# Optimization experiments

Hardware: AMD Instinct MI355X
Metric: run time of the kernel (lower is better)

## Reference

```python
import jax, jax.numpy as jnp
import numpy as np

D_MODEL = 1024
D_STATE = 16
DT_RANK = 64  # ceil(1024/16)
DT_MIN, DT_MAX = 1e-3, 1e-1


def setup_inputs() -> dict:
    key = jax.random.key(0)
    ks = jax.random.split(key, 6)
    x = jax.random.normal(ks[0], (2, 2048, D_MODEL), jnp.float32)
    A_log = jax.random.normal(ks[1], (D_MODEL, D_STATE), jnp.float32)
    D = jax.random.normal(ks[2], (D_MODEL,), jnp.float32)
    # nn.Linear default init ~ U(-1/sqrt(fan_in), 1/sqrt(fan_in)); normal*scale is fine for a baseline
    x_proj_w = jax.random.normal(ks[3], (DT_RANK + 2 * D_STATE, D_MODEL), jnp.float32) * (D_MODEL ** -0.5)
    dt_init_std = DT_RANK ** -0.5
    dt_proj_w = jax.random.uniform(ks[4], (D_MODEL, DT_RANK), jnp.float32, -dt_init_std, dt_init_std)
    dt = jnp.exp(jax.random.uniform(ks[5], (D_MODEL,), jnp.float32)
                 * (np.log(DT_MAX) - np.log(DT_MIN)) + np.log(DT_MIN))
    dt_proj_b = dt + jnp.log(-jnp.expm1(-dt))  # inverse-softplus init
    return {"x": x, "A_log": A_log, "D": D, "x_proj_w": x_proj_w,
            "dt_proj_w": dt_proj_w, "dt_proj_b": dt_proj_b}


def _s6(x, A_log, D, x_proj_w, dt_proj_w, dt_proj_b):
    A = -jnp.exp(A_log)                                    # (d, n)
    xp = jnp.einsum('bld,ed->ble', x, x_proj_w)            # (b, l, r+2n)
    d_rank = xp[..., :DT_RANK]
    Bm = xp[..., DT_RANK:DT_RANK + D_STATE]                # (b, l, n)
    Cm = xp[..., DT_RANK + D_STATE:]                       # (b, l, n)
    delta = jax.nn.softplus(jnp.einsum('blr,dr->bld', d_rank, dt_proj_w) + dt_proj_b)
    deltaA = jnp.exp(jnp.einsum('bld,dn->bldn', delta, A))          # (b, l, d, n)
    deltaB_u = jnp.einsum('bld,bln,bld->bldn', delta, Bm, x)        # (b, l, d, n)

    def step(h, inp):
        dA_t, dBu_t, C_t = inp          # (b,d,n), (b,d,n), (b,n)
        h = dA_t * h + dBu_t
        y = jnp.einsum('bdn,bn->bd', h, C_t)
        return h, y

    b, l, d = x.shape
    h0 = jnp.zeros((b, d, D_STATE), x.dtype)
    _, ys = jax.lax.scan(step, h0,
                         (deltaA.transpose(1, 0, 2, 3),
                          deltaB_u.transpose(1, 0, 2, 3),
                          Cm.transpose(1, 0, 2)))
    y = ys.transpose(1, 0, 2) + x * D                      # (b, l, d)
    return y


def reference(x, A_log, D, x_proj_w, dt_proj_w, dt_proj_b):
    return _s6(x, A_log, D, x_proj_w, dt_proj_w, dt_proj_b)
```

## Files before the change

### kernel.cpp

```cpp
#include <hip/hip_runtime.h>
#include <math.h>

#define Bb 2
#define Ll 2048
#define Dm 1024
#define Ns 16
#define Rr 64
#define Ee 96
#define XPS 8
#define BLK (Bb*Ll)
#define NTHR 256
#define LOG2E 1.4426950408889634f
#define LN2   0.6931471805599453f

__device__ inline float ex2(float x) {
#if __has_builtin(__builtin_amdgcn_exp2f)
    return __builtin_amdgcn_exp2f(x);
#else
    return exp2f(x);
#endif
}
__device__ inline float lg2(float x) {
#if __has_builtin(__builtin_amdgcn_logf)
    return __builtin_amdgcn_logf(x);
#else
    return log2f(x);
#endif
}
__device__ inline float softplus_f(float z) {
    float e = ex2(-fabsf(z) * LOG2E);
    return fmaxf(z, 0.f) + lg2(1.f + e) * LN2;
}

__global__ void __launch_bounds__(NTHR)
k_xproj(const float* __restrict__ x, const float* __restrict__ xw,
        float* __restrict__ xp_part) {
    __shared__ __align__(16) float xs[32 * 68];
    __shared__ __align__(16) float wsh[32 * 100];
    int bx = blockIdx.x;
    int ks = bx & 7, mt = bx >> 3;
    int i0 = mt * 64;
    int tid = threadIdx.x;
    int tx = tid & 15, ty = tid >> 4;
    float acc[4][6];
#pragma unroll
    for (int ii = 0; ii < 4; ++ii)
#pragma unroll
        for (int jj = 0; jj < 6; ++jj) acc[ii][jj] = 0.f;

    for (int kc = 0; kc < 4; ++kc) {
        int k0 = ks * 128 + kc * 32;
        for (int t = tid; t < 512; t += NTHR) {
            int r = t >> 3, c = (t & 7) * 4;
            float4 v = *(const float4*)(x + (size_t)(i0 + r) * Dm + k0 + c);
            xs[(c+0)*68+r] = v.x; xs[(c+1)*68+r] = v.y;
            xs[(c+2)*68+r] = v.z; xs[(c+3)*68+r] = v.w;
        }
        for (int t = tid; t < 768; t += NTHR) {
            int r = t >> 3, c = (t & 7) * 4;
            float4 v = *(const float4*)(xw + (size_t)r * Dm + k0 + c);
            wsh[(c+0)*100+r] = v.x; wsh[(c+1)*100+r] = v.y;
            wsh[(c+2)*100+r] = v.z; wsh[(c+3)*100+r] = v.w;
        }
        __syncthreads();
#pragma unroll 8
        for (int k = 0; k < 32; ++k) {
            float4 xv = *(const float4*)(xs + k*68 + ty*4);
            float2 w0 = *(const float2*)(wsh + k*100 + tx*6 + 0);
            float2 w1 = *(const float2*)(wsh + k*100 + tx*6 + 2);
            float2 w2 = *(const float2*)(wsh + k*100 + tx*6 + 4);
            float xr[4] = {xv.x, xv.y, xv.z, xv.w};
            float wr[6] = {w0.x, w0.y, w1.x, w1.y, w2.x, w2.y};
#pragma unroll
            for (int ii = 0; ii < 4; ++ii)
#pragma unroll
                for (int jj = 0; jj < 6; ++jj)
                    acc[ii][jj] = fmaf(xr[ii], wr[jj], acc[ii][jj]);
        }
        __syncthreads();
    }
#pragma unroll
    for (int ii = 0; ii < 4; ++ii)
#pragma unroll
        for (int jj = 0; jj < 6; ++jj)
            xp_part[((size_t)ks * BLK + (i0 + ty*4 + ii)) * Ee + tx*6 + jj] = acc[ii][jj];
}

__global__ void __launch_bounds__(NTHR)
k_prep(const float* __restrict__ xp_part, float* __restrict__ xp) {
    int g = blockIdx.x * NTHR + threadIdx.x;
    const float4* p = (const float4*)xp_part;
    float4 s = p[g];
#pragma unroll
    for (int i = 1; i < XPS; ++i) {
        float4 v = p[(size_t)i * (BLK * Ee / 4) + g];
        s.x += v.x; s.y += v.y; s.z += v.z; s.w += v.w;
    }
    ((float4*)xp)[g] = s;
}

__global__ void __launch_bounds__(NTHR)
k_delta(const float* __restrict__ xp, const float* __restrict__ dtw,
        const float* __restrict__ dtb, float* __restrict__ delta) {
    __shared__ __align__(16) float xs[64 * 136];
    __shared__ __align__(16) float wsh[64 * 68];
    int bx = blockIdx.x;
    int nt = bx & 15, mt = bx >> 4;
    int i0 = mt * 128, j0 = nt * 64;
    int tid = threadIdx.x, tx = tid & 15, ty = tid >> 4;

    for (int t = tid; t < 2048; t += NTHR) {
        int r = t >> 4, c = (t & 15) * 4;
        float4 v = *(const float4*)(xp + (size_t)(i0 + r) * Ee + c);
        xs[(c+0)*136+r] = v.x; xs[(c+1)*136+r] = v.y;
        xs[(c+2)*136+r] = v.z; xs[(c+3)*136+r] = v.w;
    }
    for (int t = tid; t < 1024; t += NTHR) {
        int r = t >> 4, c = (t & 15) * 4;
        float4 w = *(const float4*)(dtw + (size_t)(j0 + r) * Rr + c);
        wsh[(c+0)*68+r] = w.x; wsh[(c+1)*68+r] = w.y;
        wsh[(c+2)*68+r] = w.z; wsh[(c+3)*68+r] = w.w;
    }
    __syncthreads();

    float acc[8][4];
#pragma unroll
    for (int ii = 0; ii < 8; ++ii)
#pragma unroll
        for (int jj = 0; jj < 4; ++jj) acc[ii][jj] = 0.f;
#pragma unroll 8
    for (int k = 0; k < 64; ++k) {
        float4 xa = *(const float4*)(xs + k*136 + ty*8 + 0);
        float4 xb = *(const float4*)(xs + k*136 + ty*8 + 4);
        float4 wv = *(const float4*)(wsh + k*68 + tx*4);
        float xr[8] = {xa.x,xa.y,xa.z,xa.w, xb.x,xb.y,xb.z,xb.w};
        float wr[4] = {wv.x, wv.y, wv.z, wv.w};
#pragma unroll
        for (int ii = 0; ii < 8; ++ii)
#pragma unroll
            for (int jj = 0; jj < 4; ++jj)
                acc[ii][jj] = fmaf(xr[ii], wr[jj], acc[ii][jj]);
    }
    int d0 = j0 + tx * 4;
    float4 bias = *(const float4*)(dtb + d0);
#pragma unroll
    for (int ii = 0; ii < 8; ++ii) {
        int bl = i0 + ty*8 + ii;
        float4 o;
        o.x = softplus_f(acc[ii][0] + bias.x);
        o.y = softplus_f(acc[ii][1] + bias.y);
        o.z = softplus_f(acc[ii][2] + bias.z);
        o.w = softplus_f(acc[ii][3] + bias.w);
        *(float4*)(delta + (size_t)bl * Dm + d0) = o;
    }
}

__device__ inline void load_a2(const float* __restrict__ A_log, int d, float* a2) {
    const float4* Ap = (const float4*)(A_log + (size_t)d * Ns);
    float4 a0 = Ap[0], a1 = Ap[1], a2v = Ap[2], a3 = Ap[3];
    float tmp[Ns] = {a0.x,a0.y,a0.z,a0.w, a1.x,a1.y,a1.z,a1.w,
                     a2v.x,a2v.y,a2v.z,a2v.w, a3.x,a3.y,a3.z,a3.w};
#pragma unroll
    for (int n = 0; n < Ns; ++n) a2[n] = -__expf(tmp[n]) * LOG2E;
}

template<int CHv>
__global__ void __launch_bounds__(NTHR)
k_scan_part(const float* __restrict__ delta, const float* __restrict__ x,
            const float* __restrict__ xp, const float* __restrict__ A_log,
            float* __restrict__ Ec, float* __restrict__ Sc) {
    constexpr int CLv = Ll / CHv;
    int bx = blockIdx.x;
    int dblk = bx & 3, chunk = (bx >> 2) & (CHv - 1), b = bx >> 2 >> __builtin_ctz(CHv);
    int tid = threadIdx.x;
    int d = dblk * 256 + tid;
    int row0 = b * Ll + chunk * CLv;

    float a2[Ns], h[Ns];
    load_a2(A_log, d, a2);
#pragma unroll
    for (int n = 0; n < Ns; ++n) h[n] = 0.f;
    float sd = 0.f;

#pragma unroll 4
    for (int t = 0; t < CLv; ++t) {
        size_t row = (size_t)(row0 + t);
        float dl = delta[row * Dm + d];
        float xv = x[row * Dm + d];
        const float* bp = xp + row * Ee + Rr;
        float4 B0 = *(const float4*)(bp + 0),  B1 = *(const float4*)(bp + 4);
        float4 B2 = *(const float4*)(bp + 8),  B3 = *(const float4*)(bp + 12);
        float Bv[Ns] = {B0.x,B0.y,B0.z,B0.w, B1.x,B1.y,B1.z,B1.w,
                        B2.x,B2.y,B2.z,B2.w, B3.x,B3.y,B3.z,B3.w};
        float dx = dl * xv;
        sd += dl;
#pragma unroll
        for (int n = 0; n < Ns; ++n)
            h[n] = fmaf(ex2(dl * a2[n]), h[n], dx * Bv[n]);
    }
    size_t base = ((size_t)b * CHv + chunk) * Dm + d;
    float4* Ep = (float4*)(Ec + base * Ns);
    Ep[0] = make_float4(h[0],  h[1],  h[2],  h[3]);
    Ep[1] = make_float4(h[4],  h[5],  h[6],  h[7]);
    Ep[2] = make_float4(h[8],  h[9],  h[10], h[11]);
    Ep[3] = make_float4(h[12], h[13], h[14], h[15]);
    Sc[base] = sd;
}

template<int CHv, int G>
__global__ void __launch_bounds__(NTHR)
k_comb1(const float* __restrict__ Ec, const float* __restrict__ Sc,
        const float* __restrict__ A_log, float* __restrict__ Hloc,
        float* __restrict__ Spre, float* __restrict__ Eg, float* __restrict__ Sg) {
    constexpr int CPG = CHv / G;
    int gid = blockIdx.x * NTHR + threadIdx.x;
    int n = gid & (Ns - 1);
    int d = (gid >> 4) & (Dm - 1);
    int g = (gid >> 14) & (G - 1);
    int b = gid >> 17;
    float a2 = -__expf(A_log[d * Ns + n]) * LOG2E;
    float h = 0.f, S = 0.f;
#pragma unroll
    for (int j = 0; j < CPG; ++j) {
        size_t base = ((size_t)b * CHv + g * CPG + j) * Dm + d;
        float e  = Ec[base * Ns + n];
        float sc = Sc[base];
        Hloc[base * Ns + n] = h;
        if (n == 0) Spre[base] = S;
        h = fmaf(ex2(a2 * sc), h, e);
        S += sc;
    }
    size_t gb = ((size_t)b * G + g) * Dm + d;
    Eg[gb * Ns + n] = h;
    if (n == 0) Sg[gb] = S;
}

template<int G>
__global__ void __launch_bounds__(NTHR)
k_comb2(const float* __restrict__ Eg, const float* __restrict__ Sg,
        const float* __restrict__ A_log, float* __restrict__ Hg) {
    int gid = blockIdx.x * NTHR + threadIdx.x;
    int n = gid & (Ns - 1);
    int d = (gid >> 4) & (Dm - 1);
    int b = gid >> 14;
    float a2 = -__expf(A_log[d * Ns + n]) * LOG2E;
    float h = 0.f;
#pragma unroll
    for (int g = 0; g < G; ++g) {
        size_t gb = ((size_t)b * G + g) * Dm + d;
        Hg[gb * Ns + n] = h;
        h = fmaf(ex2(a2 * Sg[gb]), h, Eg[gb * Ns + n]);
    }
}

template<int CHv, int G>
__global__ void __launch_bounds__(NTHR)
k_scan_full(const float* __restrict__ delta, const float* __restrict__ x,
            const float* __restrict__ xp, const float* __restrict__ A_log,
            const float* __restrict__ Dp, const float* __restrict__ Hloc,
            const float* __restrict__ Spre, const float* __restrict__ Hg,
            float* __restrict__ out) {
    constexpr int CLv = Ll / CHv;
    constexpr int CPG = CHv / G;
    int bx = blockIdx.x;
    int dblk = bx & 3, chunk = (bx >> 2) & (CHv - 1), b = bx >> 2 >> __builtin_ctz(CHv);
    int tid = threadIdx.x;
    int d = dblk * 256 + tid;
    int row0 = b * Ll + chunk * CLv;

    float a2[Ns], h[Ns];
    load_a2(A_log, d, a2);
    size_t base = ((size_t)b * CHv + chunk) * Dm + d;
    size_t gb   = ((size_t)b * G + chunk / CPG) * Dm + d;
    {
        float sp = Spre[base];
        const float4* Hl = (const float4*)(Hloc + base * Ns);
        const float4* Hp = (const float4*)(Hg + gb * Ns);
        float4 l0 = Hl[0], l1 = Hl[1], l2 = Hl[2], l3 = Hl[3];
        float4 g0 = Hp[0], g1 = Hp[1], g2 = Hp[2], g3 = Hp[3];
        float lv[Ns] = {l0.x,l0.y,l0.z,l0.w, l1.x,l1.y,l1.z,l1.w,
                        l2.x,l2.y,l2.z,l2.w, l3.x,l3.y,l3.z,l3.w};
        float gv[Ns] = {g0.x,g0.y,g0.z,g0.w, g1.x,g1.y,g1.z,g1.w,
                        g2.x,g2.y,g2.z,g2.w, g3.x,g3.y,g3.z,g3.w};
#pragma unroll
        for (int n = 0; n < Ns; ++n) h[n] = fmaf(ex2(a2[n] * sp), gv[n], lv[n]);
    }
    float Dval = Dp[d];

#pragma unroll 4
    for (int t = 0; t < CLv; ++t) {
        size_t row = (size_t)(row0 + t);
        float dl = delta[row * Dm + d];
        float xv = x[row * Dm + d];
        const float* bp = xp + row * Ee + Rr;
        float4 B0 = *(const float4*)(bp + 0),  B1 = *(const float4*)(bp + 4);
        float4 B2 = *(const float4*)(bp + 8),  B3 = *(const float4*)(bp + 12);
        float4 C0 = *(const float4*)(bp + 16), C1 = *(const float4*)(bp + 20);
        float4 C2 = *(const float4*)(bp + 24), C3 = *(const float4*)(bp + 28);
        float Bv[Ns] = {B0.x,B0.y,B0.z,B0.w, B1.x,B1.y,B1.z,B1.w,
                        B2.x,B2.y,B2.z,B2.w, B3.x,B3.y,B3.z,B3.w};
        float Cv[Ns] = {C0.x,C0.y,C0.z,C0.w, C1.x,C1.y,C1.z,C1.w,
                        C2.x,C2.y,C2.z,C2.w, C3.x,C3.y,C3.z,C3.w};
        float dx = dl * xv;
        float ya[4] = {0.f, 0.f, 0.f, 0.f};
#pragma unroll
        for (int n = 0; n < Ns; ++n) {
            h[n] = fmaf(ex2(dl * a2[n]), h[n], dx * Bv[n]);
            ya[n & 3] = fmaf(h[n], Cv[n], ya[n & 3]);
        }
        out[row * Dm + d] = fmaf(xv, Dval, (ya[0] + ya[1]) + (ya[2] + ya[3]));
    }
}

extern "C" void kernel_launch(void* const* d_in, const int* in_sizes, int n_in,
                              void* d_out, int out_size, void* d_ws, size_t ws_size,
                              hipStream_t stream) {
    const float* x     = (const float*)d_in[0];
    const float* A_log = (const float*)d_in[1];
    const float* Dp    = (const float*)d_in[2];
    const float* xw    = (const float*)d_in[3];
    const float* dtw   = (const float*)d_in[4];
    const float* dtb   = (const float*)d_in[5];
    float* out = (float*)d_out;
    float* ws  = (float*)d_ws;

    float* xp      = ws;
    float* delta   = xp + 393216;
    float* S3      = delta + 4194304;
    float* xp_part = S3;

    k_xproj<<<dim3(512), dim3(NTHR), 0, stream>>>(x, xw, xp_part);
    k_prep <<<dim3(384), dim3(NTHR), 0, stream>>>(xp_part, xp);
    k_delta<<<dim3(512), dim3(NTHR), 0, stream>>>(xp, dtw, dtb, delta);

    constexpr int G = 8;
    size_t s3_128 = (size_t)Bb*128*Dm*Ns + (size_t)Bb*128*Dm + (size_t)Bb*128*Dm*Ns
                  + (size_t)Bb*128*Dm + (size_t)Bb*G*Dm*Ns + (size_t)Bb*G*Dm
                  + (size_t)Bb*G*Dm*Ns;
    size_t need128 = ((size_t)393216 + 4194304 + s3_128) * 4;
    if (ws_size >= need128) {
        constexpr int CHv = 128;
        float* Ec   = S3;
        float* Sc   = Ec   + (size_t)Bb*CHv*Dm*Ns;
        float* Hloc = Sc   + (size_t)Bb*CHv*Dm;
        float* Spre = Hloc + (size_t)Bb*CHv*Dm*Ns;
        float* Eg   = Spre + (size_t)Bb*CHv*Dm;
        float* Sg   = Eg   + (size_t)Bb*G*Dm*Ns;
        float* Hg   = Sg   + (size_t)Bb*G*Dm;
        k_scan_part<CHv>  <<<dim3(Bb*CHv*4), dim3(NTHR), 0, stream>>>(delta, x, xp, A_log, Ec, Sc);
        k_comb1<CHv, G>   <<<dim3(Bb*G*Dm*Ns/NTHR), dim3(NTHR), 0, stream>>>(Ec, Sc, A_log, Hloc, Spre, Eg, Sg);
        k_comb2<G>        <<<dim3(Bb*Dm*Ns/NTHR), dim3(NTHR), 0, stream>>>(Eg, Sg, A_log, Hg);
        k_scan_full<CHv,G><<<dim3(Bb*CHv*4), dim3(NTHR), 0, stream>>>(delta, x, xp, A_log, Dp, Hloc, Spre, Hg, out);
    } else {
        constexpr int CHv = 64;
        float* Ec   = S3;
        float* Sc   = Ec   + (size_t)Bb*CHv*Dm*Ns;
        float* Hloc = Sc   + (size_t)Bb*CHv*Dm;
        float* Spre = Hloc + (size_t)Bb*CHv*Dm*Ns;
        float* Eg   = Spre + (size_t)Bb*CHv*Dm;
        float* Sg   = Eg   + (size_t)Bb*G*Dm*Ns;
        float* Hg   = Sg   + (size_t)Bb*G*Dm;
        k_scan_part<CHv>  <<<dim3(Bb*CHv*4), dim3(NTHR), 0, stream>>>(delta, x, xp, A_log, Ec, Sc);
        k_comb1<CHv, G>   <<<dim3(Bb*G*Dm*Ns/NTHR), dim3(NTHR), 0, stream>>>(Ec, Sc, A_log, Hloc, Spre, Eg, Sg);
        k_comb2<G>        <<<dim3(Bb*Dm*Ns/NTHR), dim3(NTHR), 0, stream>>>(Eg, Sg, A_log, Hg);
        k_scan_full<CHv,G><<<dim3(Bb*CHv*4), dim3(NTHR), 0, stream>>>(delta, x, xp, A_log, Dp, Hloc, Spre, Hg, out);
    }
}
```

Measured before the change: 152.3 us.

## Fuse delta projection and softplus into both scan passes, drop delta buffer

Removes the separate k_delta GEMM kernel and the materialized delta tensor (B*L*D floats). Each scan thread now keeps its 64 dt_proj weights in registers and recomputes delta per timestep from the xp row, in both the partial and the full scan passes. This trades a 4M-float write and two reads of that tensor for twice the dot-product work and higher register pressure. The chunk count is also fixed at 64, where the code before chose 128 whenever the workspace was large enough.

```diff
diff --git a/kernel.cpp b/kernel.cpp
--- a/kernel.cpp
+++ b/kernel.cpp
@@ -99,62 +99,6 @@
     ((float4*)xp)[g] = s;
 }
 
-__global__ void __launch_bounds__(NTHR)
-k_delta(const float* __restrict__ xp, const float* __restrict__ dtw,
-        const float* __restrict__ dtb, float* __restrict__ delta) {
-    __shared__ __align__(16) float xs[64 * 136];
-    __shared__ __align__(16) float wsh[64 * 68];
-    int bx = blockIdx.x;
-    int nt = bx & 15, mt = bx >> 4;
-    int i0 = mt * 128, j0 = nt * 64;
-    int tid = threadIdx.x, tx = tid & 15, ty = tid >> 4;
-
-    for (int t = tid; t < 2048; t += NTHR) {
-        int r = t >> 4, c = (t & 15) * 4;
-        float4 v = *(const float4*)(xp + (size_t)(i0 + r) * Ee + c);
-        xs[(c+0)*136+r] = v.x; xs[(c+1)*136+r] = v.y;
-        xs[(c+2)*136+r] = v.z; xs[(c+3)*136+r] = v.w;
-    }
-    for (int t = tid; t < 1024; t += NTHR) {
-        int r = t >> 4, c = (t & 15) * 4;
-        float4 w = *(const float4*)(dtw + (size_t)(j0 + r) * Rr + c);
-        wsh[(c+0)*68+r] = w.x; wsh[(c+1)*68+r] = w.y;
-        wsh[(c+2)*68+r] = w.z; wsh[(c+3)*68+r] = w.w;
-    }
-    __syncthreads();
-
-    float acc[8][4];
-#pragma unroll
-    for (int ii = 0; ii < 8; ++ii)
-#pragma unroll
-        for (int jj = 0; jj < 4; ++jj) acc[ii][jj] = 0.f;
-#pragma unroll 8
-    for (int k = 0; k < 64; ++k) {
-        float4 xa = *(const float4*)(xs + k*136 + ty*8 + 0);
-        float4 xb = *(const float4*)(xs + k*136 + ty*8 + 4);
-        float4 wv = *(const float4*)(wsh + k*68 + tx*4);
-        float xr[8] = {xa.x,xa.y,xa.z,xa.w, xb.x,xb.y,xb.z,xb.w};
-        float wr[4] = {wv.x, wv.y, wv.z, wv.w};
-#pragma unroll
-        for (int ii = 0; ii < 8; ++ii)
-#pragma unroll
-            for (int jj = 0; jj < 4; ++jj)
-                acc[ii][jj] = fmaf(xr[ii], wr[jj], acc[ii][jj]);
-    }
-    int d0 = j0 + tx * 4;
-    float4 bias = *(const float4*)(dtb + d0);
-#pragma unroll
-    for (int ii = 0; ii < 8; ++ii) {
-        int bl = i0 + ty*8 + ii;
-        float4 o;
-        o.x = softplus_f(acc[ii][0] + bias.x);
-        o.y = softplus_f(acc[ii][1] + bias.y);
-        o.z = softplus_f(acc[ii][2] + bias.z);
-        o.w = softplus_f(acc[ii][3] + bias.w);
-        *(float4*)(delta + (size_t)bl * Dm + d0) = o;
-    }
-}
-
 __device__ inline void load_a2(const float* __restrict__ A_log, int d, float* a2) {
     const float4* Ap = (const float4*)(A_log + (size_t)d * Ns);
     float4 a0 = Ap[0], a1 = Ap[1], a2v = Ap[2], a3 = Ap[3];
@@ -164,10 +108,32 @@
     for (int n = 0; n < Ns; ++n) a2[n] = -__expf(tmp[n]) * LOG2E;
 }
 
+__device__ inline void load_w(const float* __restrict__ dtw, int d, float* w) {
+    const float4* Wp = (const float4*)(dtw + (size_t)d * Rr);
+#pragma unroll
+    for (int q = 0; q < 16; ++q) {
+        float4 v = Wp[q];
+        w[q*4+0] = v.x; w[q*4+1] = v.y; w[q*4+2] = v.z; w[q*4+3] = v.w;
+    }
+}
+
+__device__ inline float delta_of(const float* __restrict__ rp, const float* w, float bias) {
+    float z0 = bias, z1 = 0.f, z2 = 0.f, z3 = 0.f;
+#pragma unroll
+    for (int k = 0; k < 64; k += 4) {
+        z0 = fmaf(rp[k+0], w[k+0], z0);
+        z1 = fmaf(rp[k+1], w[k+1], z1);
+        z2 = fmaf(rp[k+2], w[k+2], z2);
+        z3 = fmaf(rp[k+3], w[k+3], z3);
+    }
+    return softplus_f((z0 + z1) + (z2 + z3));
+}
+
 template<int CHv>
 __global__ void __launch_bounds__(NTHR)
-k_scan_part(const float* __restrict__ delta, const float* __restrict__ x,
-            const float* __restrict__ xp, const float* __restrict__ A_log,
+k_scan_part(const float* __restrict__ x, const float* __restrict__ xp,
+            const float* __restrict__ dtw, const float* __restrict__ dtb,
+            const float* __restrict__ A_log,
             float* __restrict__ Ec, float* __restrict__ Sc) {
     constexpr int CLv = Ll / CHv;
     int bx = blockIdx.x;
@@ -176,8 +142,10 @@
     int d = dblk * 256 + tid;
     int row0 = b * Ll + chunk * CLv;
 
-    float a2[Ns], h[Ns];
+    float a2[Ns], h[Ns], w[Rr];
     load_a2(A_log, d, a2);
+    load_w(dtw, d, w);
+    float bias = dtb[d];
 #pragma unroll
     for (int n = 0; n < Ns; ++n) h[n] = 0.f;
     float sd = 0.f;
@@ -185,9 +153,10 @@
 #pragma unroll 4
     for (int t = 0; t < CLv; ++t) {
         size_t row = (size_t)(row0 + t);
-        float dl = delta[row * Dm + d];
+        const float* rp = xp + row * Ee;
+        float dl = delta_of(rp, w, bias);
         float xv = x[row * Dm + d];
-        const float* bp = xp + row * Ee + Rr;
+        const float* bp = rp + Rr;
         float4 B0 = *(const float4*)(bp + 0),  B1 = *(const float4*)(bp + 4);
         float4 B2 = *(const float4*)(bp + 8),  B3 = *(const float4*)(bp + 12);
         float Bv[Ns] = {B0.x,B0.y,B0.z,B0.w, B1.x,B1.y,B1.z,B1.w,
@@ -255,11 +224,11 @@
 
 template<int CHv, int G>
 __global__ void __launch_bounds__(NTHR)
-k_scan_full(const float* __restrict__ delta, const float* __restrict__ x,
-            const float* __restrict__ xp, const float* __restrict__ A_log,
-            const float* __restrict__ Dp, const float* __restrict__ Hloc,
-            const float* __restrict__ Spre, const float* __restrict__ Hg,
-            float* __restrict__ out) {
+k_scan_full(const float* __restrict__ x, const float* __restrict__ xp,
+            const float* __restrict__ dtw, const float* __restrict__ dtb,
+            const float* __restrict__ A_log, const float* __restrict__ Dp,
+            const float* __restrict__ Hloc, const float* __restrict__ Spre,
+            const float* __restrict__ Hg, float* __restrict__ out) {
     constexpr int CLv = Ll / CHv;
     constexpr int CPG = CHv / G;
     int bx = blockIdx.x;
@@ -268,8 +237,10 @@
     int d = dblk * 256 + tid;
     int row0 = b * Ll + chunk * CLv;
 
-    float a2[Ns], h[Ns];
+    float a2[Ns], h[Ns], w[Rr];
     load_a2(A_log, d, a2);
+    load_w(dtw, d, w);
+    float bias = dtb[d];
     size_t base = ((size_t)b * CHv + chunk) * Dm + d;
     size_t gb   = ((size_t)b * G + chunk / CPG) * Dm + d;
     {
@@ -290,9 +261,10 @@
 #pragma unroll 4
     for (int t = 0; t < CLv; ++t) {
         size_t row = (size_t)(row0 + t);
-        float dl = delta[row * Dm + d];
+        const float* rp = xp + row * Ee;
+        float dl = delta_of(rp, w, bias);
         float xv = x[row * Dm + d];
-        const float* bp = xp + row * Ee + Rr;
+        const float* bp = rp + Rr;
         float4 B0 = *(const float4*)(bp + 0),  B1 = *(const float4*)(bp + 4);
         float4 B2 = *(const float4*)(bp + 8),  B3 = *(const float4*)(bp + 12);
         float4 C0 = *(const float4*)(bp + 16), C1 = *(const float4*)(bp + 20);
@@ -325,44 +297,24 @@
     float* ws  = (float*)d_ws;
 
     float* xp      = ws;
-    float* delta   = xp + 393216;
-    float* S3      = delta + 4194304;
+    float* S3      = xp + 393216;
     float* xp_part = S3;
 
     k_xproj<<<dim3(512), dim3(NTHR), 0, stream>>>(x, xw, xp_part);
     k_prep <<<dim3(384), dim3(NTHR), 0, stream>>>(xp_part, xp);
-    k_delta<<<dim3(512), dim3(NTHR), 0, stream>>>(xp, dtw, dtb, delta);
 
     constexpr int G = 8;
-    size_t s3_128 = (size_t)Bb*128*Dm*Ns + (size_t)Bb*128*Dm + (size_t)Bb*128*Dm*Ns
-                  + (size_t)Bb*128*Dm + (size_t)Bb*G*Dm*Ns + (size_t)Bb*G*Dm
-                  + (size_t)Bb*G*Dm*Ns;
-    size_t need128 = ((size_t)393216 + 4194304 + s3_128) * 4;
-    if (ws_size >= need128) {
-        constexpr int CHv = 128;
-        float* Ec   = S3;
-        float* Sc   = Ec   + (size_t)Bb*CHv*Dm*Ns;
-        float* Hloc = Sc   + (size_t)Bb*CHv*Dm;
-        float* Spre = Hloc + (size_t)Bb*CHv*Dm*Ns;
-        float* Eg   = Spre + (size_t)Bb*CHv*Dm;
-        float* Sg   = Eg   + (size_t)Bb*G*Dm*Ns;
-        float* Hg   = Sg   + (size_t)Bb*G*Dm;
-        k_scan_part<CHv>  <<<dim3(Bb*CHv*4), dim3(NTHR), 0, stream>>>(delta, x, xp, A_log, Ec, Sc);
-        k_comb1<CHv, G>   <<<dim3(Bb*G*Dm*Ns/NTHR), dim3(NTHR), 0, stream>>>(Ec, Sc, A_log, Hloc, Spre, Eg, Sg);
-        k_comb2<G>        <<<dim3(Bb*Dm*Ns/NTHR), dim3(NTHR), 0, stream>>>(Eg, Sg, A_log, Hg);
-        k_scan_full<CHv,G><<<dim3(Bb*CHv*4), dim3(NTHR), 0, stream>>>(delta, x, xp, A_log, Dp, Hloc, Spre, Hg, out);
-    } else {
-        constexpr int CHv = 64;
-        float* Ec   = S3;
-        float* Sc   = Ec   + (size_t)Bb*CHv*Dm*Ns;
-        float* Hloc = Sc   + (size_t)Bb*CHv*Dm;
-        float* Spre = Hloc + (size_t)Bb*CHv*Dm*Ns;
-        float* Eg   = Spre + (size_t)Bb*CHv*Dm;
-        float* Sg   = Eg   + (size_t)Bb*G*Dm*Ns;
-        float* Hg   = Sg   + (size_t)Bb*G*Dm;
-        k_scan_part<CHv>  <<<dim3(Bb*CHv*4), dim3(NTHR), 0, stream>>>(delta, x, xp, A_log, Ec, Sc);
-        k_comb1<CHv, G>   <<<dim3(Bb*G*Dm*Ns/NTHR), dim3(NTHR), 0, stream>>>(Ec, Sc, A_log, Hloc, Spre, Eg, Sg);
-        k_comb2<G>        <<<dim3(Bb*Dm*Ns/NTHR), dim3(NTHR), 0, stream>>>(Eg, Sg, A_log, Hg);
-        k_scan_full<CHv,G><<<dim3(Bb*CHv*4), dim3(NTHR), 0, stream>>>(delta, x, xp, A_log, Dp, Hloc, Spre, Hg, out);
-    }
-}
+    constexpr int CHv = 64;
+    float* Ec   = S3;
+    float* Sc   = Ec   + (size_t)Bb*CHv*Dm*Ns;
+    float* Hloc = Sc   + (size_t)Bb*CHv*Dm;
+    float* Spre = Hloc + (size_t)Bb*CHv*Dm*Ns;
+    float* Eg   = Spre + (size_t)Bb*CHv*Dm;
+    float* Sg   = Eg   + (size_t)Bb*G*Dm*Ns;
+    float* Hg   = Sg   + (size_t)Bb*G*Dm;
+
+    k_scan_part<CHv>  <<<dim3(Bb*CHv*4), dim3(NTHR), 0, stream>>>(x, xp, dtw, dtb, A_log, Ec, Sc);
+    k_comb1<CHv, G>   <<<dim3(Bb*G*Dm*Ns/NTHR), dim3(NTHR), 0, stream>>>(Ec, Sc, A_log, Hloc, Spre, Eg, Sg);
+    k_comb2<G>        <<<dim3(Bb*Dm*Ns/NTHR), dim3(NTHR), 0, stream>>>(Eg, Sg, A_log, Hg);
+    k_scan_full<CHv,G><<<dim3(Bb*CHv*4), dim3(NTHR), 0, stream>>>(x, xp, dtw, dtb, A_log, Dp, Hloc, Spre, Hg, out);
+}
```

Measured after the change: 188.6 us. +23.8%, slower.

## Split each channel's 16 states across two threads in chunked scan kernels

Applied to the files above, without the earlier changes.

The two scan kernels now give each thread one half of the 16-state vector of a channel, so twice as many threads cover the same channels. Partial outputs are combined with a lane shuffle. Launch bounds now request more waves per CU, and the CH=128 path is dropped in favour of a fixed CH=64 chunking. This lowers register pressure and raises parallelism. In exchange, each thread reloads delta and x redundantly and pays a shuffle per timestep.

```diff
diff --git a/kernel.cpp b/kernel.cpp
--- a/kernel.cpp
+++ b/kernel.cpp
@@ -155,31 +155,31 @@
     }
 }
 
-__device__ inline void load_a2(const float* __restrict__ A_log, int d, float* a2) {
-    const float4* Ap = (const float4*)(A_log + (size_t)d * Ns);
-    float4 a0 = Ap[0], a1 = Ap[1], a2v = Ap[2], a3 = Ap[3];
-    float tmp[Ns] = {a0.x,a0.y,a0.z,a0.w, a1.x,a1.y,a1.z,a1.w,
-                     a2v.x,a2v.y,a2v.z,a2v.w, a3.x,a3.y,a3.z,a3.w};
-#pragma unroll
-    for (int n = 0; n < Ns; ++n) a2[n] = -__expf(tmp[n]) * LOG2E;
+__device__ inline void load_a2h(const float* __restrict__ A_log, int d, int half, float* a2) {
+    const float4* Ap = (const float4*)(A_log + (size_t)d * Ns + half * 8);
+    float4 a0 = Ap[0], a1 = Ap[1];
+    float tmp[8] = {a0.x,a0.y,a0.z,a0.w, a1.x,a1.y,a1.z,a1.w};
+#pragma unroll
+    for (int n = 0; n < 8; ++n) a2[n] = -__expf(tmp[n]) * LOG2E;
 }
 
 template<int CHv>
-__global__ void __launch_bounds__(NTHR)
+__global__ void __launch_bounds__(NTHR, 4)
 k_scan_part(const float* __restrict__ delta, const float* __restrict__ x,
             const float* __restrict__ xp, const float* __restrict__ A_log,
             float* __restrict__ Ec, float* __restrict__ Sc) {
     constexpr int CLv = Ll / CHv;
     int bx = blockIdx.x;
-    int dblk = bx & 3, chunk = (bx >> 2) & (CHv - 1), b = bx >> 2 >> __builtin_ctz(CHv);
+    int dblk = bx & 7, chunk = (bx >> 3) & (CHv - 1), b = bx >> (3 + __builtin_ctz(CHv));
     int tid = threadIdx.x;
-    int d = dblk * 256 + tid;
+    int half = tid & 1;
+    int d = dblk * 128 + (tid >> 1);
     int row0 = b * Ll + chunk * CLv;
 
-    float a2[Ns], h[Ns];
-    load_a2(A_log, d, a2);
-#pragma unroll
-    for (int n = 0; n < Ns; ++n) h[n] = 0.f;
+    float a2[8], h[8];
+    load_a2h(A_log, d, half, a2);
+#pragma unroll
+    for (int n = 0; n < 8; ++n) h[n] = 0.f;
     float sd = 0.f;
 
 #pragma unroll 4
@@ -187,23 +187,19 @@
         size_t row = (size_t)(row0 + t);
         float dl = delta[row * Dm + d];
         float xv = x[row * Dm + d];
-        const float* bp = xp + row * Ee + Rr;
-        float4 B0 = *(const float4*)(bp + 0),  B1 = *(const float4*)(bp + 4);
-        float4 B2 = *(const float4*)(bp + 8),  B3 = *(const float4*)(bp + 12);
-        float Bv[Ns] = {B0.x,B0.y,B0.z,B0.w, B1.x,B1.y,B1.z,B1.w,
-                        B2.x,B2.y,B2.z,B2.w, B3.x,B3.y,B3.z,B3.w};
+        const float* bp = xp + row * Ee + Rr + half * 8;
+        float4 B0 = *(const float4*)(bp + 0), B1 = *(const float4*)(bp + 4);
+        float Bv[8] = {B0.x,B0.y,B0.z,B0.w, B1.x,B1.y,B1.z,B1.w};
         float dx = dl * xv;
         sd += dl;
 #pragma unroll
-        for (int n = 0; n < Ns; ++n)
+        for (int n = 0; n < 8; ++n)
             h[n] = fmaf(ex2(dl * a2[n]), h[n], dx * Bv[n]);
     }
     size_t base = ((size_t)b * CHv + chunk) * Dm + d;
-    float4* Ep = (float4*)(Ec + base * Ns);
-    Ep[0] = make_float4(h[0],  h[1],  h[2],  h[3]);
-    Ep[1] = make_float4(h[4],  h[5],  h[6],  h[7]);
-    Ep[2] = make_float4(h[8],  h[9],  h[10], h[11]);
-    Ep[3] = make_float4(h[12], h[13], h[14], h[15]);
+    float4* Ep = (float4*)(Ec + base * Ns + half * 8);
+    Ep[0] = make_float4(h[0], h[1], h[2], h[3]);
+    Ep[1] = make_float4(h[4], h[5], h[6], h[7]);
     Sc[base] = sd;
 }
 
@@ -254,7 +250,7 @@
 }
 
 template<int CHv, int G>
-__global__ void __launch_bounds__(NTHR)
+__global__ void __launch_bounds__(NTHR, 4)
 k_scan_full(const float* __restrict__ delta, const float* __restrict__ x,
             const float* __restrict__ xp, const float* __restrict__ A_log,
             const float* __restrict__ Dp, const float* __restrict__ Hloc,
@@ -263,27 +259,26 @@
     constexpr int CLv = Ll / CHv;
     constexpr int CPG = CHv / G;
     int bx = blockIdx.x;
-    int dblk = bx & 3, chunk = (bx >> 2) & (CHv - 1), b = bx >> 2 >> __builtin_ctz(CHv);
+    int dblk = bx & 7, chunk = (bx >> 3) & (CHv - 1), b = bx >> (3 + __builtin_ctz(CHv));
     int tid = threadIdx.x;
-    int d = dblk * 256 + tid;
+    int half = tid & 1;
+    int d = dblk * 128 + (tid >> 1);
     int row0 = b * Ll + chunk * CLv;
 
-    float a2[Ns], h[Ns];
-    load_a2(A_log, d, a2);
+    float a2[8], h[8];
+    load_a2h(A_log, d, half, a2);
     size_t base = ((size_t)b * CHv + chunk) * Dm + d;
     size_t gb   = ((size_t)b * G + chunk / CPG) * Dm + d;
     {
         float sp = Spre[base];
-        const float4* Hl = (const float4*)(Hloc + base * Ns);
-        const float4* Hp = (const float4*)(Hg + gb * Ns);
-        float4 l0 = Hl[0], l1 = Hl[1], l2 = Hl[2], l3 = Hl[3];
-        float4 g0 = Hp[0], g1 = Hp[1], g2 = Hp[2], g3 = Hp[3];
-        float lv[Ns] = {l0.x,l0.y,l0.z,l0.w, l1.x,l1.y,l1.z,l1.w,
-                        l2.x,l2.y,l2.z,l2.w, l3.x,l3.y,l3.z,l3.w};
-        float gv[Ns] = {g0.x,g0.y,g0.z,g0.w, g1.x,g1.y,g1.z,g1.w,
-                        g2.x,g2.y,g2.z,g2.w, g3.x,g3.y,g3.z,g3.w};
-#pragma unroll
-        for (int n = 0; n < Ns; ++n) h[n] = fmaf(ex2(a2[n] * sp), gv[n], lv[n]);
+        const float4* Hl = (const float4*)(Hloc + base * Ns + half * 8);
+        const float4* Hp = (const float4*)(Hg + gb * Ns + half * 8);
+        float4 l0 = Hl[0], l1 = Hl[1];
+        float4 g0 = Hp[0], g1 = Hp[1];
+        float lv[8] = {l0.x,l0.y,l0.z,l0.w, l1.x,l1.y,l1.z,l1.w};
+        float gv[8] = {g0.x,g0.y,g0.z,g0.w, g1.x,g1.y,g1.z,g1.w};
+#pragma unroll
+        for (int n = 0; n < 8; ++n) h[n] = fmaf(ex2(a2[n] * sp), gv[n], lv[n]);
     }
     float Dval = Dp[d];
 
@@ -292,23 +287,21 @@
         size_t row = (size_t)(row0 + t);
         float dl = delta[row * Dm + d];
         float xv = x[row * Dm + d];
-        const float* bp = xp + row * Ee + Rr;
+        const float* bp = xp + row * Ee + Rr + half * 8;
         float4 B0 = *(const float4*)(bp + 0),  B1 = *(const float4*)(bp + 4);
-        float4 B2 = *(const float4*)(bp + 8),  B3 = *(const float4*)(bp + 12);
         float4 C0 = *(const float4*)(bp + 16), C1 = *(const float4*)(bp + 20);
-        float4 C2 = *(const float4*)(bp + 24), C3 = *(const float4*)(bp + 28);
-        float Bv[Ns] = {B0.x,B0.y,B0.z,B0.w, B1.x,B1.y,B1.z,B1.w,
-                        B2.x,B2.y,B2.z,B2.w, B3.x,B3.y,B3.z,B3.w};
-        float Cv[Ns] = {C0.x,C0.y,C0.z,C0.w, C1.x,C1.y,C1.z,C1.w,
-                        C2.x,C2.y,C2.z,C2.w, C3.x,C3.y,C3.z,C3.w};
+        float Bv[8] = {B0.x,B0.y,B0.z,B0.w, B1.x,B1.y,B1.z,B1.w};
+        float Cv[8] = {C0.x,C0.y,C0.z,C0.w, C1.x,C1.y,C1.z,C1.w};
         float dx = dl * xv;
         float ya[4] = {0.f, 0.f, 0.f, 0.f};
 #pragma unroll
-        for (int n = 0; n < Ns; ++n) {
+        for (int n = 0; n < 8; ++n) {
             h[n] = fmaf(ex2(dl * a2[n]), h[n], dx * Bv[n]);
             ya[n & 3] = fmaf(h[n], Cv[n], ya[n & 3]);
         }
-        out[row * Dm + d] = fmaf(xv, Dval, (ya[0] + ya[1]) + (ya[2] + ya[3]));
+        float ys = (ya[0] + ya[1]) + (ya[2] + ya[3]);
+        ys += __shfl_xor(ys, 1);
+        out[row * Dm + d] = fmaf(xv, Dval, ys);
     }
 }
 
@@ -334,35 +327,17 @@
     k_delta<<<dim3(512), dim3(NTHR), 0, stream>>>(xp, dtw, dtb, delta);
 
     constexpr int G = 8;
-    size_t s3_128 = (size_t)Bb*128*Dm*Ns + (size_t)Bb*128*Dm + (size_t)Bb*128*Dm*Ns
-                  + (size_t)Bb*128*Dm + (size_t)Bb*G*Dm*Ns + (size_t)Bb*G*Dm
-                  + (size_t)Bb*G*Dm*Ns;
-    size_t need128 = ((size_t)393216 + 4194304 + s3_128) * 4;
-    if (ws_size >= need128) {
-        constexpr int CHv = 128;
-        float* Ec   = S3;
-        float* Sc   = Ec   + (size_t)Bb*CHv*Dm*Ns;
-        float* Hloc = Sc   + (size_t)Bb*CHv*Dm;
-        float* Spre = Hloc + (size_t)Bb*CHv*Dm*Ns;
-        float* Eg   = Spre + (size_t)Bb*CHv*Dm;
-        float* Sg   = Eg   + (size_t)Bb*G*Dm*Ns;
-        float* Hg   = Sg   + (size_t)Bb*G*Dm;
-        k_scan_part<CHv>  <<<dim3(Bb*CHv*4), dim3(NTHR), 0, stream>>>(delta, x, xp, A_log, Ec, Sc);
-        k_comb1<CHv, G>   <<<dim3(Bb*G*Dm*Ns/NTHR), dim3(NTHR), 0, stream>>>(Ec, Sc, A_log, Hloc, Spre, Eg, Sg);
-        k_comb2<G>        <<<dim3(Bb*Dm*Ns/NTHR), dim3(NTHR), 0, stream>>>(Eg, Sg, A_log, Hg);
-        k_scan_full<CHv,G><<<dim3(Bb*CHv*4), dim3(NTHR), 0, stream>>>(delta, x, xp, A_log, Dp, Hloc, Spre, Hg, out);
-    } else {
-        constexpr int CHv = 64;
-        float* Ec   = S3;
-        float* Sc   = Ec   + (size_t)Bb*CHv*Dm*Ns;
-        float* Hloc = Sc   + (size_t)Bb*CHv*Dm;
-        float* Spre = Hloc + (size_t)Bb*CHv*Dm*Ns;
-        float* Eg   = Spre + (size_t)Bb*CHv*Dm;
-        float* Sg   = Eg   + (size_t)Bb*G*Dm*Ns;
-        float* Hg   = Sg   + (size_t)Bb*G*Dm;
-        k_scan_part<CHv>  <<<dim3(Bb*CHv*4), dim3(NTHR), 0, stream>>>(delta, x, xp, A_log, Ec, Sc);
-        k_comb1<CHv, G>   <<<dim3(Bb*G*Dm*Ns/NTHR), dim3(NTHR), 0, stream>>>(Ec, Sc, A_log, Hloc, Spre, Eg, Sg);
-        k_comb2<G>        <<<dim3(Bb*Dm*Ns/NTHR), dim3(NTHR), 0, stream>>>(Eg, Sg, A_log, Hg);
-        k_scan_full<CHv,G><<<dim3(Bb*CHv*4), dim3(NTHR), 0, stream>>>(delta, x, xp, A_log, Dp, Hloc, Spre, Hg, out);
-    }
-}
+    constexpr int CHv = 64;
+    float* Ec   = S3;
+    float* Sc   = Ec   + (size_t)Bb*CHv*Dm*Ns;
+    float* Hloc = Sc   + (size_t)Bb*CHv*Dm;
+    float* Spre = Hloc + (size_t)Bb*CHv*Dm*Ns;
+    float* Eg   = Spre + (size_t)Bb*CHv*Dm;
+    float* Sg   = Eg   + (size_t)Bb*G*Dm*Ns;
+    float* Hg   = Sg   + (size_t)Bb*G*Dm;
+
+    k_scan_part<CHv>  <<<dim3(Bb*CHv*8), dim3(NTHR), 0, stream>>>(delta, x, xp, A_log, Ec, Sc);
+    k_comb1<CHv, G>   <<<dim3(Bb*G*Dm*Ns/NTHR), dim3(NTHR), 0, stream>>>(Ec, Sc, A_log, Hloc, Spre, Eg, Sg);
+    k_comb2<G>        <<<dim3(Bb*Dm*Ns/NTHR), dim3(NTHR), 0, stream>>>(Eg, Sg, A_log, Hg);
+    k_scan_full<CHv,G><<<dim3(Bb*CHv*8), dim3(NTHR), 0, stream>>>(delta, x, xp, A_log, Dp, Hloc, Spre, Hg, out);
+}
```

Measured after the change: 157.4 us. 3.4% more time.
